# Performance work log

Hardware: AMD Instinct MI355X
Metric: run time of the kernel (lower is better)

Reference implementation:

```python
import jax, jax.numpy as jnp
import numpy as np

N = 50000          # num_entities
R = 16             # num_relations
D = 128            # embedding_dim
B = 4              # num_blocks
d = D // B         # block size (32)
E = 800000         # num edges


def setup_inputs() -> dict:
    key = jax.random.key(0)
    ks = jax.random.split(key, 9)
    s = 1.0 / np.sqrt(D)
    return {
        "edge_index": jax.random.randint(ks[0], (2, E), 0, N),
        "edge_type": jax.random.randint(ks[1], (E,), 0, R),
        "node_emb": jax.random.normal(ks[2], (N, D), jnp.float32) * s,
        "W1": jax.random.normal(ks[3], (R, B, d, d), jnp.float32) * s,
        "root1": jax.random.normal(ks[4], (D, D), jnp.float32) * s,
        "bias1": jax.random.normal(ks[5], (D,), jnp.float32) * 0.01,
        "W2": jax.random.normal(ks[6], (R, B, d, d), jnp.float32) * s,
        "root2": jax.random.normal(ks[7], (D, D), jnp.float32) * s,
        "bias2": jax.random.normal(ks[8], (D,), jnp.float32) * 0.01,
    }


def _rgcn_conv(x, src, dst, et, W, root, bias):
    # x: [N, D]; W: [R, B, d, d] block-diagonal per-relation weights.
    n = x.shape[0]
    # Transform every node under every relation (cheaper than gathering
    # per-edge weight blocks): [R, N, B, d] -> [R, N, D]
    allR = jnp.einsum('nbi,rbio->rnbo', x.reshape(n, B, d), W).reshape(R, n, D)
    msg = allR[et, src]                                   # [E, D] gather
    # Per-relation mean normalization 1/c_{i,r} (PyG RGCNConv aggr='mean'
    # applied per relation): count edges per (dst, relation) pair.
    seg = dst * R + et
    cnt = jax.ops.segment_sum(jnp.ones_like(et, x.dtype), seg, num_segments=n * R)
    norm = 1.0 / jnp.maximum(cnt[seg], 1.0)               # [E]
    agg = jax.ops.segment_sum(msg * norm[:, None], dst, num_segments=n)
    return agg + x @ root + bias


def reference(edge_index, edge_type, node_emb, W1, root1, bias1, W2, root2, bias2):
    src, dst = edge_index[0], edge_index[1]
    h = _rgcn_conv(node_emb, src, dst, edge_type, W1, root1, bias1)
    h = jax.nn.relu(h)  # dropout is identity in eval mode
    return _rgcn_conv(h, src, dst, edge_type, W2, root2, bias2)
```

## Files before the change

kernel.cpp:

```cpp
#include <hip/hip_runtime.h>
#include <hip/hip_bf16.h>

#define N_NODES 50000
#define N_REL   16
#define DIM     128
#define NBLK    4
#define BS      32
#define N_EDGES 800000
#define NSEG    (N_NODES * N_REL)
#define SCAN_BLK 1024
#define N_SCAN_BLKS ((NSEG + SCAN_BLK - 1) / SCAN_BLK)
#define NWT     (N_NODES / 16)

typedef __attribute__((ext_vector_type(8))) short s8v;
typedef __attribute__((ext_vector_type(8))) unsigned short u8v;
typedef __attribute__((ext_vector_type(4))) float f4v;

__device__ __forceinline__ float bf2f(unsigned short u) {
    return __uint_as_float(((unsigned int)u) << 16);
}
__device__ __forceinline__ unsigned short f2bfbits(float f) {
    unsigned int u = __float_as_uint(f);
    return (unsigned short)((u + 0x7fffu + ((u >> 16) & 1u)) >> 16);
}

__global__ __launch_bounds__(256) void count_kernel(const int* __restrict__ dst,
                                                    const int* __restrict__ et,
                                                    int* __restrict__ cnt, int E) {
    int e = blockIdx.x * 256 + threadIdx.x;
    if (e < E) atomicAdd(&cnt[dst[e] * N_REL + et[e]], 1);
}

__global__ __launch_bounds__(256) void scan1_kernel(const int* __restrict__ in,
                                                    int* __restrict__ out,
                                                    int* __restrict__ bsum, int M) {
    const int t = threadIdx.x;
    const int base = blockIdx.x * SCAN_BLK + t * 4;
    int v0 = (base + 0 < M) ? in[base + 0] : 0;
    int v1 = (base + 1 < M) ? in[base + 1] : 0;
    int v2 = (base + 2 < M) ? in[base + 2] : 0;
    int v3 = (base + 3 < M) ? in[base + 3] : 0;
    const int s = v0 + v1 + v2 + v3;
    const int lane = t & 63, wid = t >> 6;
    int inc = s;
    for (int d = 1; d < 64; d <<= 1) {
        int u = __shfl_up(inc, d, 64);
        if (lane >= d) inc += u;
    }
    __shared__ int wsum[5];
    if (lane == 63) wsum[wid] = inc;
    __syncthreads();
    if (t == 0) {
        int a = 0;
        for (int w = 0; w < 4; ++w) { int u = wsum[w]; wsum[w] = a; a += u; }
        wsum[4] = a;
    }
    __syncthreads();
    const int ex = inc - s + wsum[wid];
    if (base + 0 < M) out[base + 0] = ex;
    if (base + 1 < M) out[base + 1] = ex + v0;
    if (base + 2 < M) out[base + 2] = ex + v0 + v1;
    if (base + 3 < M) out[base + 3] = ex + v0 + v1 + v2;
    if (t == 0) bsum[blockIdx.x] = wsum[4];
}

__global__ __launch_bounds__(1024) void scan2_kernel(int* __restrict__ bsum, int nb) {
    const int t = threadIdx.x;
    int s = (t < nb) ? bsum[t] : 0;
    const int lane = t & 63, wid = t >> 6;
    int inc = s;
    for (int d = 1; d < 64; d <<= 1) {
        int u = __shfl_up(inc, d, 64);
        if (lane >= d) inc += u;
    }
    __shared__ int wsum[16];
    if (lane == 63) wsum[wid] = inc;
    __syncthreads();
    if (t == 0) {
        int a = 0;
        for (int w = 0; w < 16; ++w) { int u = wsum[w]; wsum[w] = a; a += u; }
    }
    __syncthreads();
    const int ex = inc - s + wsum[wid];
    if (t < nb) bsum[t] = ex;
}

__global__ __launch_bounds__(256) void scan3_kernel(int* __restrict__ out,
                                                    const int* __restrict__ bsum, int M) {
    int i = blockIdx.x * 256 + threadIdx.x;
    if (i < M) out[i] += bsum[i / SCAN_BLK];
}

__global__ __launch_bounds__(256) void scatter_fast_kernel(const int* __restrict__ src,
                                                           const int* __restrict__ dst,
                                                           const int* __restrict__ et,
                                                           int* __restrict__ off,
                                                           const int* __restrict__ cnt,
                                                           int2* __restrict__ evec, int E) {
    int e = blockIdx.x * 256 + threadIdx.x;
    if (e < E) {
        int r = et[e];
        int seg = dst[e] * N_REL + r;
        int pos = atomicAdd(&off[seg], 1);
        float inv = 1.0f / (float)cnt[seg];
        evec[pos] = make_int2(r * N_NODES + src[e], __float_as_int(inv));
    }
}

__global__ __launch_bounds__(256) void scatter_old_kernel(const int* __restrict__ src,
                                                          const int* __restrict__ dst,
                                                          const int* __restrict__ et,
                                                          int* __restrict__ off,
                                                          int* __restrict__ srcs, int E) {
    int e = blockIdx.x * 256 + threadIdx.x;
    if (e < E) {
        int seg = dst[e] * N_REL + et[e];
        int pos = atomicAdd(&off[seg], 1);
        srcs[pos] = src[e];
    }
}

__global__ __launch_bounds__(256) void prep_kernel(const float* __restrict__ W1,
                                                   const float* __restrict__ W2,
                                                   const float* __restrict__ r1,
                                                   const float* __restrict__ r2,
                                                   ushort* __restrict__ WB1,
                                                   ushort* __restrict__ WB2,
                                                   ushort* __restrict__ RB1,
                                                   ushort* __restrict__ RB2) {
    int t = blockIdx.x * 256 + threadIdx.x;
    if (t < 262144) {
        const float* W = (t < 131072) ? W1 : W2;
        ushort* WB     = (t < 131072) ? WB1 : WB2;
        int idx = t & 131071;
        int i  = idx & 7;
        int lm = (idx >> 3) & 15;
        int kg = (idx >> 7) & 3;
        int mt = (idx >> 9) & 1;
        int b  = (idx >> 10) & 3;
        int r  = idx >> 12;
        WB[idx] = f2bfbits(W[((size_t)(r * 4 + b) * 32 + kg * 8 + i) * 32 + mt * 16 + lm]);
    } else if (t < 294912) {
        int u = t - 262144;
        const float* R = (u < 16384) ? r1 : r2;
        ushort* RB     = (u < 16384) ? RB1 : RB2;
        int idx = u & 16383;
        int i  = idx & 7;
        int lm = (idx >> 3) & 15;
        int kg = (idx >> 7) & 3;
        int kc = (idx >> 9) & 3;
        int mt = (idx >> 11) & 7;
        RB[idx] = f2bfbits(R[(size_t)(kc * 32 + kg * 8 + i) * DIM + mt * 16 + lm]);
    }
}

template<bool IN_BF16, bool RELU>
__global__ __launch_bounds__(256) void allr8_kernel(const void* __restrict__ xin,
                                                    const ushort* __restrict__ WB,
                                                    char* __restrict__ tab,
                                                    float* __restrict__ scl) {
    const int wv = threadIdx.x >> 6;
    const int l  = threadIdx.x & 63;
    const int wt = blockIdx.x * 4 + wv;
    if (wt >= NWT) return;
    const int rg = blockIdx.y;
    const int nbase = wt * 16;
    const int lm = l & 15;
    const int kg = l >> 4;
    const int node = nbase + lm;

    s8v bfr[4];
#pragma unroll
    for (int b = 0; b < 4; ++b) {
        if (IN_BF16) {
            const ushort* xp = (const ushort*)xin + (size_t)node * DIM + b * BS + kg * 8;
            u8v u = *(const u8v*)xp;
#pragma unroll
            for (int i = 0; i < 8; ++i) {
                unsigned short us = u[i];
                if (RELU) us = (us & 0x8000u) ? (unsigned short)0 : us;
                bfr[b][i] = (short)us;
            }
        } else {
            const float* xp = (const float*)xin + (size_t)node * DIM + b * BS + kg * 8;
#pragma unroll
            for (int i = 0; i < 8; ++i) {
                float v = xp[i];
                if (RELU) v = fmaxf(v, 0.f);
                bfr[b][i] = (short)f2bfbits(v);
            }
        }
    }

    for (int ri = 0; ri < 4; ++ri) {
        const int rr = rg * 4 + ri;
        f4v acc[4][2];
#pragma unroll
        for (int b = 0; b < 4; ++b) {
#pragma unroll
            for (int mt = 0; mt < 2; ++mt) {
                s8v afrag = *(const s8v*)&WB[((((rr * 4 + b) * 2 + mt) * 4 + kg) * 16 + lm) * 8];
                f4v z = {0.f, 0.f, 0.f, 0.f};
                acc[b][mt] = __builtin_amdgcn_mfma_f32_16x16x32_bf16(afrag, bfr[b], z, 0, 0, 0);
            }
        }
        float m = 0.f;
#pragma unroll
        for (int b = 0; b < 4; ++b)
#pragma unroll
            for (int mt = 0; mt < 2; ++mt)
#pragma unroll
                for (int j = 0; j < 4; ++j)
                    m = fmaxf(m, fabsf(acc[b][mt][j]));
        m = fmaxf(m, __shfl_xor(m, 16, 64));
        m = fmaxf(m, __shfl_xor(m, 32, 64));
        m = fmaxf(m, 1e-30f);
        const float qs = 127.0f / m;

        unsigned int d[8];
#pragma unroll
        for (int b = 0; b < 4; ++b) {
#pragma unroll
            for (int mt = 0; mt < 2; ++mt) {
                int q0 = __float2int_rn(acc[b][mt][0] * qs);
                int q1 = __float2int_rn(acc[b][mt][1] * qs);
                int q2 = __float2int_rn(acc[b][mt][2] * qs);
                int q3 = __float2int_rn(acc[b][mt][3] * qs);
                unsigned int t01 = __builtin_amdgcn_perm((unsigned)q1, (unsigned)q0, 0x00000400u);
                unsigned int t23 = __builtin_amdgcn_perm((unsigned)q3, (unsigned)q2, 0x00000400u);
                d[b * 2 + mt] = __builtin_amdgcn_perm(t23, t01, 0x05040100u);
            }
        }
        char* gp = tab + ((size_t)rr * N_NODES + node) * 128 + kg * 32;
        *(uint4*)gp        = make_uint4(d[0], d[1], d[2], d[3]);
        *(uint4*)(gp + 16) = make_uint4(d[4], d[5], d[6], d[7]);
        if (kg == 0) scl[rr * N_NODES + node] = m * (1.0f / 127.0f);
    }
}

template<bool IN_BF16, bool OUT_BF16, bool RELU>
__global__ __launch_bounds__(256) void dense_rb_kernel(const void* __restrict__ xin,
                                                       const ushort* __restrict__ RB,
                                                       const float* __restrict__ bias,
                                                       void* __restrict__ outv) {
    const int wv = threadIdx.x >> 6;
    const int l  = threadIdx.x & 63;
    const int wt = blockIdx.x * 4 + wv;
    if (wt >= NWT) return;
    const int nbase = wt * 16;
    const int lm = l & 15;
    const int kg = l >> 4;
    const int node = nbase + lm;

    s8v bfr[4];
#pragma unroll
    for (int kc = 0; kc < 4; ++kc) {
        if (IN_BF16) {
            const ushort* xp = (const ushort*)xin + (size_t)node * DIM + kc * BS + kg * 8;
            u8v u = *(const u8v*)xp;
#pragma unroll
            for (int i = 0; i < 8; ++i) {
                unsigned short us = u[i];
                if (RELU) us = (us & 0x8000u) ? (unsigned short)0 : us;
                bfr[kc][i] = (short)us;
            }
        } else {
            const float* xp = (const float*)xin + (size_t)node * DIM + kc * BS + kg * 8;
#pragma unroll
            for (int i = 0; i < 8; ++i) {
                float v = xp[i];
                if (RELU) v = fmaxf(v, 0.f);
                bfr[kc][i] = (short)f2bfbits(v);
            }
        }
    }
#pragma unroll 2
    for (int mt = 0; mt < 8; ++mt) {
        const int col0 = mt * 16 + kg * 4;
        f4v acc = *(const f4v*)&bias[col0];
#pragma unroll
        for (int kc = 0; kc < 4; ++kc) {
            s8v afrag = *(const s8v*)&RB[(((mt * 4 + kc) * 4 + kg) * 16 + lm) * 8];
            acc = __builtin_amdgcn_mfma_f32_16x16x32_bf16(afrag, bfr[kc], acc, 0, 0, 0);
        }
        if (OUT_BF16) {
            unsigned int p0 = (unsigned int)f2bfbits(acc[0]) |
                              ((unsigned int)f2bfbits(acc[1]) << 16);
            unsigned int p1 = (unsigned int)f2bfbits(acc[2]) |
                              ((unsigned int)f2bfbits(acc[3]) << 16);
            *(uint2*)((ushort*)outv + (size_t)node * DIM + col0) = make_uint2(p0, p1);
        } else {
            *(f4v*)((float*)outv + (size_t)node * DIM + col0) = acc;
        }
    }
}

template<bool OUT_BF16>
__global__ __launch_bounds__(256) void agg8_kernel(const int2* __restrict__ evec,
                                                   const int* __restrict__ off,
                                                   const char* __restrict__ tab,
                                                   const float* __restrict__ scl,
                                                   void* __restrict__ outv) {
    const int hw = threadIdx.x >> 5;
    const int o  = threadIdx.x & 31;
    const int v  = blockIdx.x * 8 + hw;

    const int start = (v == 0) ? 0 : off[v * N_REL - 1];
    const int end   = off[v * N_REL + N_REL - 1];

    const int p = o >> 4;
    const int w = o & 15;

    float acc[8];
#pragma unroll
    for (int j = 0; j < 8; ++j) acc[j] = 0.f;

    for (int base = start; base < end; base += 4) {
        const int k0 = base + p;
        const int k1 = base + 2 + p;
        const int2 e0 = evec[min(k0, end - 1)];
        const int2 e1 = evec[min(k1, end - 1)];
        const int g0 = e0.x, g1 = e1.x;
        const float i0 = (k0 < end) ? __int_as_float(e0.y) : 0.f;
        const float i1 = (k1 < end) ? __int_as_float(e1.y) : 0.f;
        const uint2 q0 = *(const uint2*)(tab + (size_t)g0 * 128 + w * 8);
        const uint2 q1 = *(const uint2*)(tab + (size_t)g1 * 128 + w * 8);
        const float s0 = scl[g0] * i0;
        const float s1 = scl[g1] * i1;
#pragma unroll
        for (int j = 0; j < 4; ++j) {
            acc[j]     = fmaf((float)(int)(signed char)(q0.x >> (8 * j)), s0, acc[j]);
            acc[4 + j] = fmaf((float)(int)(signed char)(q0.y >> (8 * j)), s0, acc[4 + j]);
        }
#pragma unroll
        for (int j = 0; j < 4; ++j) {
            acc[j]     = fmaf((float)(int)(signed char)(q1.x >> (8 * j)), s1, acc[j]);
            acc[4 + j] = fmaf((float)(int)(signed char)(q1.y >> (8 * j)), s1, acc[4 + j]);
        }
    }
#pragma unroll
    for (int j = 0; j < 8; ++j)
        acc[j] += __shfl_xor(acc[j], 16, 32);

    if (o < 16) {
        const int base0 = (o & 3) * 32 + (o >> 2) * 4;
        if (OUT_BF16) {
            ushort* hp = (ushort*)outv + (size_t)v * DIM + base0;
            ushort4 a0 = *(ushort4*)hp;
            ushort4 a1 = *(ushort4*)(hp + 16);
            a0.x = f2bfbits(bf2f(a0.x) + acc[0]);
            a0.y = f2bfbits(bf2f(a0.y) + acc[1]);
            a0.z = f2bfbits(bf2f(a0.z) + acc[2]);
            a0.w = f2bfbits(bf2f(a0.w) + acc[3]);
            a1.x = f2bfbits(bf2f(a1.x) + acc[4]);
            a1.y = f2bfbits(bf2f(a1.y) + acc[5]);
            a1.z = f2bfbits(bf2f(a1.z) + acc[6]);
            a1.w = f2bfbits(bf2f(a1.w) + acc[7]);
            *(ushort4*)hp        = a0;
            *(ushort4*)(hp + 16) = a1;
        } else {
            float* op = (float*)outv + (size_t)v * DIM + base0;
            float4 r0 = *(float4*)op;
            float4 r1 = *(float4*)(op + 16);
            r0.x += acc[0]; r0.y += acc[1]; r0.z += acc[2]; r0.w += acc[3];
            r1.x += acc[4]; r1.y += acc[5]; r1.z += acc[6]; r1.w += acc[7];
            *(float4*)op        = r0;
            *(float4*)(op + 16) = r1;
        }
    }
}

template<bool RELU>
__global__ __launch_bounds__(256) void dense_old_kernel(const float* __restrict__ x,
                                                        const float* __restrict__ root,
                                                        const float* __restrict__ bias,
                                                        float* __restrict__ out) {
    const int wv = threadIdx.x >> 6;
    const int l  = threadIdx.x & 63;
    const int wt = blockIdx.x * 4 + wv;
    if (wt >= NWT) return;
    const int nbase = wt * 16;
    const int lm = l & 15;
    const int kg = l >> 4;
    const int node = nbase + lm;

    s8v bfr[4];
#pragma unroll
    for (int kc = 0; kc < 4; ++kc) {
        const float* xp = &x[(size_t)node * DIM + kc * BS + kg * 8];
#pragma unroll
        for (int i = 0; i < 8; ++i) {
            float v = xp[i];
            if (RELU) v = fmaxf(v, 0.f);
            bfr[kc][i] = (short)f2bfbits(v);
        }
    }
#pragma unroll 2
    for (int mt = 0; mt < 8; ++mt) {
        const int col0 = mt * 16 + kg * 4;
        f4v acc = *(const f4v*)&bias[col0];
#pragma unroll
        for (int kc = 0; kc < 4; ++kc) {
            const float* rp = &root[(size_t)(kc * BS + kg * 8) * DIM + mt * 16 + lm];
            s8v afrag;
#pragma unroll
            for (int i = 0; i < 8; ++i)
                afrag[i] = (short)f2bfbits(rp[i * DIM]);
            acc = __builtin_amdgcn_mfma_f32_16x16x32_bf16(afrag, bfr[kc], acc, 0, 0, 0);
        }
        *(f4v*)&out[(size_t)node * DIM + col0] = acc;
    }
}

template<bool RELU>
__global__ __launch_bounds__(256) void agg_fallback_kernel(const int* __restrict__ srcs,
                                                           const int* __restrict__ off,
                                                           const int* __restrict__ cnt,
                                                           const float* __restrict__ x,
                                                           const float* __restrict__ W,
                                                           float* __restrict__ out) {
    __shared__ float Wsh[N_REL * BS * BS];
    const int bblk = blockIdx.y;
    for (int idx = threadIdx.x * 4; idx < N_REL * BS * BS; idx += 1024) {
        int r = idx >> 10, rest = idx & 1023;
        *(float4*)&Wsh[idx] = *(const float4*)&W[(r * NBLK + bblk) * 1024 + rest];
    }
    __syncthreads();
    const int hw = threadIdx.x >> 5;
    const int o  = threadIdx.x & 31;
    const int v  = blockIdx.x * 8 + hw;
    int endv = 0, cv = 0;
    if (o < N_REL) { endv = off[v * N_REL + o]; cv = cnt[v * N_REL + o]; }
    float acc = out[v * DIM + bblk * BS + o];
    for (int r = 0; r < N_REL; ++r) {
        const int c = __shfl(cv, r, 32);
        if (c == 0) continue;
        const int end = __shfl(endv, r, 32);
        float xs = 0.f;
        for (int k = end - c; k < end; ++k) {
            const int s = srcs[k];
            float xv = x[s * DIM + bblk * BS + o];
            if (RELU) xv = fmaxf(xv, 0.f);
            xs += xv;
        }
        xs *= (1.0f / (float)c);
        const float* wr = &Wsh[r * (BS * BS)];
#pragma unroll
        for (int i = 0; i < BS; i += 2) {
            float xi0 = __shfl(xs, i, 32);
            float xi1 = __shfl(xs, i + 1, 32);
            acc = fmaf(xi0, wr[i * BS + o], acc);
            acc = fmaf(xi1, wr[(i + 1) * BS + o], acc);
        }
    }
    out[v * DIM + bblk * BS + o] = acc;
}

extern "C" void kernel_launch(void* const* d_in, const int* in_sizes, int n_in,
                              void* d_out, int out_size, void* d_ws, size_t ws_size,
                              hipStream_t stream) {
    const int*   edge_index = (const int*)d_in[0];
    const int*   src   = edge_index;
    const int*   dstv  = edge_index + N_EDGES;
    const int*   et    = (const int*)d_in[1];
    const float* x0    = (const float*)d_in[2];
    const float* W1    = (const float*)d_in[3];
    const float* root1 = (const float*)d_in[4];
    const float* bias1 = (const float*)d_in[5];
    const float* W2    = (const float*)d_in[6];
    const float* root2 = (const float*)d_in[7];
    const float* bias2 = (const float*)d_in[8];
    float* out = (float*)d_out;

    char* ws = (char*)d_ws;
    ushort* h    = (ushort*)ws;
    int*    cnt  = (int*)   (ws + 12800000);
    int*    off  = (int*)   (ws + 16000000);
    int2*   evec = (int2*)  (ws + 19200000);
    int*    bsum = (int*)   (ws + 25600000);
    ushort* WB1  = (ushort*)(ws + 25604096);
    ushort* WB2  = (ushort*)(ws + 25866240);
    ushort* RB1  = (ushort*)(ws + 26128384);
    ushort* RB2  = (ushort*)(ws + 26161152);
    float*  scl  = (float*) (ws + 26193920);
    char*   tab  =          (ws + 29393920);
    const size_t FAST_NEED = 131793920ull;

    const int egrid = (N_EDGES + 255) / 256;
    const int tgrid = (NWT + 3) / 4;

    if (ws_size >= FAST_NEED) {
        prep_kernel<<<1152, 256, 0, stream>>>(W1, W2, root1, root2, WB1, WB2, RB1, RB2);
        hipMemsetAsync(cnt, 0, (size_t)NSEG * sizeof(int), stream);
        count_kernel<<<egrid, 256, 0, stream>>>(dstv, et, cnt, N_EDGES);
        scan1_kernel<<<N_SCAN_BLKS, 256, 0, stream>>>(cnt, off, bsum, NSEG);
        scan2_kernel<<<1, 1024, 0, stream>>>(bsum, N_SCAN_BLKS);
        scan3_kernel<<<(NSEG + 255) / 256, 256, 0, stream>>>(off, bsum, NSEG);
        scatter_fast_kernel<<<egrid, 256, 0, stream>>>(src, dstv, et, off, cnt, evec, N_EDGES);

        dim3 agrid_r(tgrid, 4);
        const int ngrid = N_NODES / 8;

        dense_rb_kernel<false, true, false><<<tgrid, 256, 0, stream>>>(x0, RB1, bias1, h);
        allr8_kernel<false, false><<<agrid_r, 256, 0, stream>>>(x0, WB1, tab, scl);
        agg8_kernel<true><<<ngrid, 256, 0, stream>>>(evec, off, tab, scl, h);

        dense_rb_kernel<true, false, true><<<tgrid, 256, 0, stream>>>(h, RB2, bias2, out);
        allr8_kernel<true, true><<<agrid_r, 256, 0, stream>>>(h, WB2, tab, scl);
        agg8_kernel<false><<<ngrid, 256, 0, stream>>>(evec, off, tab, scl, out);
    } else {
        float* hf    = (float*)d_ws;
        int*   cntf  = (int*)((char*)d_ws + 25600000);
        int*   offf  = (int*)((char*)d_ws + 28800000);
        int*   srcsf = (int*)((char*)d_ws + 32000000);
        int*   bsumf = (int*)((char*)d_ws + 35200000);

        hipMemsetAsync(cntf, 0, (size_t)NSEG * sizeof(int), stream);
        count_kernel<<<egrid, 256, 0, stream>>>(dstv, et, cntf, N_EDGES);
        scan1_kernel<<<N_SCAN_BLKS, 256, 0, stream>>>(cntf, offf, bsumf, NSEG);
        scan2_kernel<<<1, 1024, 0, stream>>>(bsumf, N_SCAN_BLKS);
        scan3_kernel<<<(NSEG + 255) / 256, 256, 0, stream>>>(offf, bsumf, NSEG);
        scatter_old_kernel<<<egrid, 256, 0, stream>>>(src, dstv, et, offf, srcsf, N_EDGES);

        dim3 fgrid(N_NODES / 8, NBLK);
        dense_old_kernel<false><<<tgrid, 256, 0, stream>>>(x0, root1, bias1, hf);
        agg_fallback_kernel<false><<<fgrid, 256, 0, stream>>>(srcsf, offf, cntf, x0, W1, hf);
        dense_old_kernel<true><<<tgrid, 256, 0, stream>>>(hf, root2, bias2, out);
        agg_fallback_kernel<true><<<fgrid, 256, 0, stream>>>(srcsf, offf, cntf, hf, W2, out);
    }
}
```

Before: 273.5 us.

## Fuse root dense transform into per-relation table kernel, unroll aggregation loop

Merges the dense root/bias kernel and the per-relation int8 table kernel into one kernel that loads each node tile's input fragments once and then runs all 16 relations plus the root projection. This removes a launch per layer and a second read of the input activations. In exchange the grid shrinks by a factor of four (relations are no longer split across blockIdx.y), so each wave does more serial work and there is less parallelism and possibly more register pressure. The edge aggregation loop also gets an unroll-by-2 pragma to expose more gather loads in flight.

Result: faster. 253.4 us (-7.3%).

```diff
diff --git a/kernel.cpp b/kernel.cpp
--- a/kernel.cpp
+++ b/kernel.cpp
@@ -154,16 +154,18 @@
     }
 }
 
-template<bool IN_BF16, bool RELU>
-__global__ __launch_bounds__(256) void allr8_kernel(const void* __restrict__ xin,
+template<bool IN_BF16, bool OUT_BF16, bool RELU>
+__global__ __launch_bounds__(256) void fused_kernel(const void* __restrict__ xin,
                                                     const ushort* __restrict__ WB,
+                                                    const ushort* __restrict__ RB,
+                                                    const float* __restrict__ bias,
                                                     char* __restrict__ tab,
-                                                    float* __restrict__ scl) {
+                                                    float* __restrict__ scl,
+                                                    void* __restrict__ outv) {
     const int wv = threadIdx.x >> 6;
     const int l  = threadIdx.x & 63;
     const int wt = blockIdx.x * 4 + wv;
     if (wt >= NWT) return;
-    const int rg = blockIdx.y;
     const int nbase = wt * 16;
     const int lm = l & 15;
     const int kg = l >> 4;
@@ -192,8 +194,8 @@
         }
     }
 
-    for (int ri = 0; ri < 4; ++ri) {
-        const int rr = rg * 4 + ri;
+#pragma unroll 2
+    for (int rr = 0; rr < N_REL; ++rr) {
         f4v acc[4][2];
 #pragma unroll
         for (int b = 0; b < 4; ++b) {
@@ -236,44 +238,7 @@
         *(uint4*)(gp + 16) = make_uint4(d[4], d[5], d[6], d[7]);
         if (kg == 0) scl[rr * N_NODES + node] = m * (1.0f / 127.0f);
     }
-}
-
-template<bool IN_BF16, bool OUT_BF16, bool RELU>
-__global__ __launch_bounds__(256) void dense_rb_kernel(const void* __restrict__ xin,
-                                                       const ushort* __restrict__ RB,
-                                                       const float* __restrict__ bias,
-                                                       void* __restrict__ outv) {
-    const int wv = threadIdx.x >> 6;
-    const int l  = threadIdx.x & 63;
-    const int wt = blockIdx.x * 4 + wv;
-    if (wt >= NWT) return;
-    const int nbase = wt * 16;
-    const int lm = l & 15;
-    const int kg = l >> 4;
-    const int node = nbase + lm;
-
-    s8v bfr[4];
-#pragma unroll
-    for (int kc = 0; kc < 4; ++kc) {
-        if (IN_BF16) {
-            const ushort* xp = (const ushort*)xin + (size_t)node * DIM + kc * BS + kg * 8;
-            u8v u = *(const u8v*)xp;
-#pragma unroll
-            for (int i = 0; i < 8; ++i) {
-                unsigned short us = u[i];
-                if (RELU) us = (us & 0x8000u) ? (unsigned short)0 : us;
-                bfr[kc][i] = (short)us;
-            }
-        } else {
-            const float* xp = (const float*)xin + (size_t)node * DIM + kc * BS + kg * 8;
-#pragma unroll
-            for (int i = 0; i < 8; ++i) {
-                float v = xp[i];
-                if (RELU) v = fmaxf(v, 0.f);
-                bfr[kc][i] = (short)f2bfbits(v);
-            }
-        }
-    }
+
 #pragma unroll 2
     for (int mt = 0; mt < 8; ++mt) {
         const int col0 = mt * 16 + kg * 4;
@@ -315,6 +280,7 @@
 #pragma unroll
     for (int j = 0; j < 8; ++j) acc[j] = 0.f;
 
+#pragma unroll 2
     for (int base = start; base < end; base += 4) {
         const int k0 = base + p;
         const int k1 = base + 2 + p;
@@ -498,15 +464,14 @@
         scan3_kernel<<<(NSEG + 255) / 256, 256, 0, stream>>>(off, bsum, NSEG);
         scatter_fast_kernel<<<egrid, 256, 0, stream>>>(src, dstv, et, off, cnt, evec, N_EDGES);
 
-        dim3 agrid_r(tgrid, 4);
         const int ngrid = N_NODES / 8;
 
-        dense_rb_kernel<false, true, false><<<tgrid, 256, 0, stream>>>(x0, RB1, bias1, h);
-        allr8_kernel<false, false><<<agrid_r, 256, 0, stream>>>(x0, WB1, tab, scl);
+        fused_kernel<false, true, false><<<tgrid, 256, 0, stream>>>(
+            x0, WB1, RB1, bias1, tab, scl, h);
         agg8_kernel<true><<<ngrid, 256, 0, stream>>>(evec, off, tab, scl, h);
 
-        dense_rb_kernel<true, false, true><<<tgrid, 256, 0, stream>>>(h, RB2, bias2, out);
-        allr8_kernel<true, true><<<agrid_r, 256, 0, stream>>>(h, WB2, tab, scl);
+        fused_kernel<true, false, true><<<tgrid, 256, 0, stream>>>(
+            h, WB2, RB2, bias2, tab, scl, out);
         agg8_kernel<false><<<ngrid, 256, 0, stream>>>(evec, off, tab, scl, out);
     } else {
         float* hf    = (float*)d_ws;
```
